# Optimization experiments

Hardware: AMD Instinct MI355X
Metric: run time of the kernel (lower is better)

Reference implementation:

```python
import jax, jax.numpy as jnp
import numpy as np


def _grid_sample_3d(vol, grid):
    """Trilinear 3D grid_sample, zero padding, align_corners=False (torch default).

    vol:  [B, C, D, H, W]
    grid: [B, P, 3] normalized coords in [-1, 1]; grid[...,0]->W axis,
          grid[...,1]->H axis, grid[...,2]->D axis (torch convention).
    returns [B, C, P]
    """
    B, C, D, H, W = vol.shape
    x = (grid[..., 0] + 1.0) * (W * 0.5) - 0.5
    y = (grid[..., 1] + 1.0) * (H * 0.5) - 0.5
    z = (grid[..., 2] + 1.0) * (D * 0.5) - 0.5
    x0, y0, z0 = jnp.floor(x), jnp.floor(y), jnp.floor(z)
    gather = jax.vmap(lambda v, zz, yy, xx: v[:, zz, yy, xx])  # per-batch gather -> [C, P]
    out = jnp.zeros((B, C, x.shape[1]), vol.dtype)
    for dz in (0.0, 1.0):
        for dy in (0.0, 1.0):
            for dx in (0.0, 1.0):
                xi, yi, zi = x0 + dx, y0 + dy, z0 + dz
                w = (1.0 - jnp.abs(x - xi)) * (1.0 - jnp.abs(y - yi)) * (1.0 - jnp.abs(z - zi))
                valid = (xi >= 0) & (xi < W) & (yi >= 0) & (yi < H) & (zi >= 0) & (zi < D)
                xc = jnp.clip(xi, 0, W - 1).astype(jnp.int32)
                yc = jnp.clip(yi, 0, H - 1).astype(jnp.int32)
                zc = jnp.clip(zi, 0, D - 1).astype(jnp.int32)
                vals = gather(vol, zc, yc, xc)  # [B, C, P]
                out = out + vals * jnp.where(valid, w, 0.0)[:, None, :]
    return out


def _offset_grid(xs, A, Wk):
    """xs: [N,3] sample points; A: [N,3,3]; Wk: [3,K] offset weights.
    Returns [N, K, 3] grid coords ordered (z_feat, y_feat, x_feat) as in the torch code."""
    off = jnp.einsum('nij,jk->nik', A, Wk)  # bmm with repeated weight -> [N,3,K]
    xf = xs[:, 2:3] + off[:, 0, :]
    yf = xs[:, 1:2] + off[:, 1, :]
    zf = xs[:, 0:1] + off[:, 2, :]
    return jnp.stack([zf, yf, xf], axis=-1)


def setup_inputs() -> dict:
    key = jax.random.key(0)
    k1, k2, k3, k4 = jax.random.split(key, 4)
    B, C, D, H, W = 2, 16, 96, 96, 96
    Feats, K = 512, 1024
    inp = jax.random.normal(k1, (B, C, D, H, W), jnp.float32)
    xyz_sample = jax.random.uniform(k2, (B, Feats, 3), jnp.float32, -1.0, 1.0)
    A = jax.random.normal(k3, (B * Feats, 3, 3), jnp.float32) * 0.1
    weight = jax.random.normal(k4, (6, K), jnp.float32) * 0.05  # xyz_off.weight
    return {"input": inp, "xyz_sample": xyz_sample, "A": A, "weight": weight}


def reference(input, xyz_sample, A, weight):
    B, Feats, _ = xyz_sample.shape
    C = input.shape[1]
    K = weight.shape[1]  # 1024
    xs = xyz_sample.reshape(B * Feats, 3)
    g1 = _offset_grid(xs, A, weight[:3]).reshape(B, Feats * K, 3)
    g2 = _offset_grid(xs, A, weight[3:]).reshape(B, Feats * K, 3)
    feats = _grid_sample_3d(input, g1) - _grid_sample_3d(input, g2)  # [B, C, Feats*K]
    return feats.reshape(B, C * Feats, K)
```

## Files before the change

kernel.cpp:

```cpp
#include <hip/hip_runtime.h>


#define NB 2
#define NC 16
#define NS 96
#define FEATS 512
#define NK 1024
#define KSPLIT 4
#define KSHIFT 2
#define KCHUNK (NK / KSPLIT)
#define PASSES (KCHUNK / 64)

#define TP 388

__device__ __forceinline__ unsigned int bfround(float f) {
  unsigned int u = __float_as_uint(f);
  return (u + 0x7fffu + ((u >> 16) & 1u)) >> 16;
}

__global__ __launch_bounds__(256) void transpose_bf16_kernel(
    const float* __restrict__ vol, unsigned short* __restrict__ volT) {
  int bid = blockIdx.x;
  int hq = bid % 24;
  int t = bid / 24;
  int d = t % NS;
  int b = t / NS;

  __shared__ float sm[NC * TP];
  int tid = threadIdx.x;

  const float4* v4 = (const float4*)vol;
#pragma unroll
  for (int j = 0; j < 6; j++) {
    int i = tid + 256 * j;
    int c = i / 96;
    int u = i - c * 96;
    size_t src = (size_t)((b * NC + c) * NS + d) * 2304 + hq * 96 + u;
    *(float4*)&sm[c * TP + u * 4] = v4[src];
  }
  __syncthreads();

  size_t dstb = ((size_t)(b * NS + d) * 9216 + (size_t)hq * 384) * NC;
#pragma unroll
  for (int j = 0; j < 3; j++) {
    int m = tid + 256 * j;
    int t16 = m >> 1;
    int ch = m & 1;
    unsigned int r[4];
#pragma unroll
    for (int q = 0; q < 4; q++) {
      float lo = sm[(ch * 8 + 2 * q) * TP + t16];
      float hi = sm[(ch * 8 + 2 * q + 1) * TP + t16];
      r[q] = bfround(lo) | (bfround(hi) << 16);
    }
    *(uint4*)(volT + dstb + (size_t)m * 8) = make_uint4(r[0], r[1], r[2], r[3]);
  }
}

__device__ __forceinline__ void tri_q_bf16(const unsigned short* __restrict__ vq,
                                           size_t bbase, float x, float y,
                                           float z, float sgn, float acc[4]) {
  float fx0 = floorf(x), fy0 = floorf(y), fz0 = floorf(z);
  int ix0 = (int)fx0, iy0 = (int)fy0, iz0 = (int)fz0;
  float tx = x - fx0, ty = y - fy0, tz = z - fz0;
  float wxa[2] = {1.0f - tx, tx};
  float wya[2] = {1.0f - ty, ty};
  float wza[2] = {1.0f - tz, tz};

#pragma unroll
  for (int dz = 0; dz < 2; dz++) {
    int zc = iz0 + dz;
    if ((unsigned)zc >= (unsigned)NS) continue;
#pragma unroll
    for (int dy = 0; dy < 2; dy++) {
      int yc = iy0 + dy;
      if ((unsigned)yc >= (unsigned)NS) continue;
      size_t rowb = bbase + ((size_t)zc * NS + yc) * (NS * NC);
      float wzy = sgn * wza[dz] * wya[dy];
#pragma unroll
      for (int dx = 0; dx < 2; dx++) {
        int xc = ix0 + dx;
        if ((unsigned)xc >= (unsigned)NS) continue;
        float w = wzy * wxa[dx];
        uint2 u = *(const uint2*)(vq + rowb + (size_t)xc * NC);
        acc[0] += w * __uint_as_float(u.x << 16);
        acc[1] += w * __uint_as_float(u.x & 0xffff0000u);
        acc[2] += w * __uint_as_float(u.y << 16);
        acc[3] += w * __uint_as_float(u.y & 0xffff0000u);
      }
    }
  }
}

__global__ __launch_bounds__(256) void sample_kernel_q(
    const unsigned short* __restrict__ volT,
    const float* __restrict__ xyz, const float* __restrict__ A,
    const float* __restrict__ weight, float* __restrict__ out) {
  __shared__ float wsm[6 * KCHUNK];

  int bid = blockIdx.x;
  int kseg = bid & (KSPLIT - 1);
  int n = bid >> KSHIFT;
  int b = n >> 9;
  int f = n & 511;
  int kbase = kseg * KCHUNK;

  for (int i = threadIdx.x; i < 6 * KCHUNK; i += 256)
    wsm[i] = weight[(i / KCHUNK) * NK + kbase + (i % KCHUNK)];

  const float* An = A + (size_t)n * 9;
  float a00 = An[0], a01 = An[1], a02 = An[2];
  float a10 = An[3], a11 = An[4], a12 = An[5];
  float a20 = An[6], a21 = An[7], a22 = An[8];
  const float* Xn = xyz + (size_t)n * 3;
  float bx = (Xn[0] + 1.0f) * 48.0f - 0.5f;
  float by = (Xn[1] + 1.0f) * 48.0f - 0.5f;
  float bz = (Xn[2] + 1.0f) * 48.0f - 0.5f;
  __syncthreads();

  int quad = threadIdx.x & 3;
  int ksub = threadIdx.x >> 2;
  const unsigned short* vq = volT + quad * 4;
  size_t bbase = (size_t)b * (NS * NS * NS * NC);
  size_t obase = (size_t)b * (NC * FEATS * NK) +
                 (size_t)(quad * 4) * (FEATS * NK) + (size_t)f * NK + kbase;

  for (int pass = 0; pass < PASSES; pass++) {
    int kl = pass * 64 + ksub;
    float w0 = wsm[kl];
    float w1 = wsm[KCHUNK + kl];
    float w2 = wsm[2 * KCHUNK + kl];
    float w3 = wsm[3 * KCHUNK + kl];
    float w4 = wsm[4 * KCHUNK + kl];
    float w5 = wsm[5 * KCHUNK + kl];

    float acc[4] = {0.0f, 0.0f, 0.0f, 0.0f};

    {
      float oz = a00 * w0 + a01 * w1 + a02 * w2;
      float oy = a10 * w0 + a11 * w1 + a12 * w2;
      float ox = a20 * w0 + a21 * w1 + a22 * w2;
      tri_q_bf16(vq, bbase, bx + ox * 48.0f, by + oy * 48.0f, bz + oz * 48.0f,
                 1.0f, acc);
    }
    {
      float oz = a00 * w3 + a01 * w4 + a02 * w5;
      float oy = a10 * w3 + a11 * w4 + a12 * w5;
      float ox = a20 * w3 + a21 * w4 + a22 * w5;
      tri_q_bf16(vq, bbase, bx + ox * 48.0f, by + oy * 48.0f, bz + oz * 48.0f,
                 -1.0f, acc);
    }

    size_t o = obase + kl;
    out[o] = acc[0];
    out[o + (size_t)(FEATS * NK)] = acc[1];
    out[o + 2 * (size_t)(FEATS * NK)] = acc[2];
    out[o + 3 * (size_t)(FEATS * NK)] = acc[3];
  }
}

__global__ __launch_bounds__(256) void sample_kernel_fallback(
    const float* __restrict__ vol, const float* __restrict__ xyz,
    const float* __restrict__ A, const float* __restrict__ weight,
    float* __restrict__ out) {
  int n = blockIdx.x;
  int b = n >> 9;
  int f = n & 511;
  const float* An = A + (size_t)n * 9;
  float a00 = An[0], a01 = An[1], a02 = An[2];
  float a10 = An[3], a11 = An[4], a12 = An[5];
  float a20 = An[6], a21 = An[7], a22 = An[8];
  const float* Xn = xyz + (size_t)n * 3;
  float bx = (Xn[0] + 1.0f) * 48.0f - 0.5f;
  float by = (Xn[1] + 1.0f) * 48.0f - 0.5f;
  float bz = (Xn[2] + 1.0f) * 48.0f - 0.5f;
  size_t obase = (size_t)b * (NC * FEATS * NK) + (size_t)f * NK;

  for (int k = threadIdx.x; k < NK; k += 256) {
    float w0 = weight[k], w1 = weight[NK + k], w2 = weight[2 * NK + k];
    float w3 = weight[3 * NK + k], w4 = weight[4 * NK + k],
          w5 = weight[5 * NK + k];
    float acc[NC];
#pragma unroll
    for (int c = 0; c < NC; c++) acc[c] = 0.0f;
    for (int g = 0; g < 2; g++) {
      float u0 = g ? w3 : w0, u1 = g ? w4 : w1, u2 = g ? w5 : w2;
      float sgn = g ? -1.0f : 1.0f;
      float oz = a00 * u0 + a01 * u1 + a02 * u2;
      float oy = a10 * u0 + a11 * u1 + a12 * u2;
      float ox = a20 * u0 + a21 * u1 + a22 * u2;
      float x = bx + ox * 48.0f, y = by + oy * 48.0f, z = bz + oz * 48.0f;
      float fx0 = floorf(x), fy0 = floorf(y), fz0 = floorf(z);
      int ix0 = (int)fx0, iy0 = (int)fy0, iz0 = (int)fz0;
      float tx = x - fx0, ty = y - fy0, tz = z - fz0;
      float wxa[2] = {1.0f - tx, tx}, wya[2] = {1.0f - ty, ty},
            wza[2] = {1.0f - tz, tz};
      for (int dz = 0; dz < 2; dz++) {
        int zc = iz0 + dz;
        if ((unsigned)zc >= (unsigned)NS) continue;
        for (int dy = 0; dy < 2; dy++) {
          int yc = iy0 + dy;
          if ((unsigned)yc >= (unsigned)NS) continue;
          for (int dx = 0; dx < 2; dx++) {
            int xc = ix0 + dx;
            if ((unsigned)xc >= (unsigned)NS) continue;
            float w = sgn * wza[dz] * wya[dy] * wxa[dx];
            size_t base = (size_t)b * NC * NS * NS * NS +
                          (size_t)zc * NS * NS + (size_t)yc * NS + xc;
#pragma unroll
            for (int c = 0; c < NC; c++)
              acc[c] += w * vol[base + (size_t)c * (NS * NS * NS)];
          }
        }
      }
    }
#pragma unroll
    for (int c = 0; c < NC; c++)
      out[obase + (size_t)c * (FEATS * NK) + k] = acc[c];
  }
}

extern "C" void kernel_launch(void* const* d_in, const int* in_sizes, int n_in,
                              void* d_out, int out_size, void* d_ws,
                              size_t ws_size, hipStream_t stream) {
  const float* vol    = (const float*)d_in[0];
  const float* xyz    = (const float*)d_in[1];
  const float* A      = (const float*)d_in[2];
  const float* weight = (const float*)d_in[3];
  float* out = (float*)d_out;

  const size_t volT_bytes =
      (size_t)NB * NC * NS * NS * NS * sizeof(unsigned short);

  if (ws_size >= volT_bytes) {
    unsigned short* volT = (unsigned short*)d_ws;
    transpose_bf16_kernel<<<NB * NS * 24, 256, 0, stream>>>(vol, volT);
    sample_kernel_q<<<NB * FEATS * KSPLIT, 256, 0, stream>>>(volT, xyz, A,
                                                             weight, out);
  } else {
    sample_kernel_fallback<<<NB * FEATS, 256, 0, stream>>>(vol, xyz, A, weight,
                                                           out);
  }
}
```

Before: 242.2 us.

## Stage local 8x8x8 voxel neighborhood in LDS and split channels across two threads

```diff
diff --git a/kernel.cpp b/kernel.cpp
--- a/kernel.cpp
+++ b/kernel.cpp
@@ -9,7 +9,10 @@
 #define KSPLIT 4
 #define KSHIFT 2
 #define KCHUNK (NK / KSPLIT)
-#define PASSES (KCHUNK / 64)
+#define DPASSES (KCHUNK / 128)
+
+#define RVOX 8
+#define VSTRIDE 48
 
 #define TP 388
 
@@ -57,9 +60,15 @@
   }
 }
 
-__device__ __forceinline__ void tri_q_bf16(const unsigned short* __restrict__ vq,
-                                           size_t bbase, float x, float y,
-                                           float z, float sgn, float acc[4]) {
+#define BLO(v) __uint_as_float((v) << 16)
+#define BHI(v) __uint_as_float((v) & 0xffff0000u)
+
+__device__ __forceinline__ void tri_duo(
+    const unsigned short* __restrict__ vg,
+    size_t bbase,
+    const unsigned char* __restrict__ sp,
+    int ox0, int oy0, int oz0,
+    float x, float y, float z, float sgn, float acc[8]) {
   float fx0 = floorf(x), fy0 = floorf(y), fz0 = floorf(z);
   int ix0 = (int)fx0, iy0 = (int)fy0, iz0 = (int)fz0;
   float tx = x - fx0, ty = y - fy0, tz = z - fz0;
@@ -67,26 +76,59 @@
   float wya[2] = {1.0f - ty, ty};
   float wza[2] = {1.0f - tz, tz};
 
-#pragma unroll
-  for (int dz = 0; dz < 2; dz++) {
-    int zc = iz0 + dz;
-    if ((unsigned)zc >= (unsigned)NS) continue;
-#pragma unroll
-    for (int dy = 0; dy < 2; dy++) {
-      int yc = iy0 + dy;
-      if ((unsigned)yc >= (unsigned)NS) continue;
-      size_t rowb = bbase + ((size_t)zc * NS + yc) * (NS * NC);
-      float wzy = sgn * wza[dz] * wya[dy];
-#pragma unroll
-      for (int dx = 0; dx < 2; dx++) {
-        int xc = ix0 + dx;
-        if ((unsigned)xc >= (unsigned)NS) continue;
-        float w = wzy * wxa[dx];
-        uint2 u = *(const uint2*)(vq + rowb + (size_t)xc * NC);
-        acc[0] += w * __uint_as_float(u.x << 16);
-        acc[1] += w * __uint_as_float(u.x & 0xffff0000u);
-        acc[2] += w * __uint_as_float(u.y << 16);
-        acc[3] += w * __uint_as_float(u.y & 0xffff0000u);
+  int lx0 = ix0 - ox0, ly0 = iy0 - oy0, lz0 = iz0 - oz0;
+  bool fast = ((unsigned)lx0 < 7u) & ((unsigned)ly0 < 7u) & ((unsigned)lz0 < 7u);
+
+  if (__builtin_expect(fast, 1)) {
+#pragma unroll
+    for (int dz = 0; dz < 2; dz++) {
+      float wz = sgn * wza[dz];
+#pragma unroll
+      for (int dy = 0; dy < 2; dy++) {
+        float wzy = wz * wya[dy];
+        const unsigned char* rp =
+            sp + (((lz0 + dz) * RVOX + (ly0 + dy)) * RVOX + lx0) * VSTRIDE;
+#pragma unroll
+        for (int dx = 0; dx < 2; dx++) {
+          float w = wzy * wxa[dx];
+          uint4 u = *(const uint4*)(rp + dx * VSTRIDE);
+          acc[0] += w * BLO(u.x);
+          acc[1] += w * BHI(u.x);
+          acc[2] += w * BLO(u.y);
+          acc[3] += w * BHI(u.y);
+          acc[4] += w * BLO(u.z);
+          acc[5] += w * BHI(u.z);
+          acc[6] += w * BLO(u.w);
+          acc[7] += w * BHI(u.w);
+        }
+      }
+    }
+  } else {
+#pragma unroll
+    for (int dz = 0; dz < 2; dz++) {
+      int zc = iz0 + dz;
+      if ((unsigned)zc >= (unsigned)NS) continue;
+#pragma unroll
+      for (int dy = 0; dy < 2; dy++) {
+        int yc = iy0 + dy;
+        if ((unsigned)yc >= (unsigned)NS) continue;
+        size_t rowb = bbase + ((size_t)zc * NS + yc) * (NS * NC);
+        float wzy = sgn * wza[dz] * wya[dy];
+#pragma unroll
+        for (int dx = 0; dx < 2; dx++) {
+          int xc = ix0 + dx;
+          if ((unsigned)xc >= (unsigned)NS) continue;
+          float w = wzy * wxa[dx];
+          uint4 u = *(const uint4*)(vg + rowb + (size_t)xc * NC);
+          acc[0] += w * BLO(u.x);
+          acc[1] += w * BHI(u.x);
+          acc[2] += w * BLO(u.y);
+          acc[3] += w * BHI(u.y);
+          acc[4] += w * BLO(u.z);
+          acc[5] += w * BHI(u.z);
+          acc[6] += w * BLO(u.w);
+          acc[7] += w * BHI(u.w);
+        }
       }
     }
   }
@@ -97,6 +139,7 @@
     const float* __restrict__ xyz, const float* __restrict__ A,
     const float* __restrict__ weight, float* __restrict__ out) {
   __shared__ float wsm[6 * KCHUNK];
+  __shared__ __align__(16) unsigned char stage[RVOX * RVOX * RVOX * VSTRIDE];
 
   int bid = blockIdx.x;
   int kseg = bid & (KSPLIT - 1);
@@ -116,17 +159,40 @@
   float bx = (Xn[0] + 1.0f) * 48.0f - 0.5f;
   float by = (Xn[1] + 1.0f) * 48.0f - 0.5f;
   float bz = (Xn[2] + 1.0f) * 48.0f - 0.5f;
+
+  int ox0 = (int)floorf(bx) - 3;
+  int oy0 = (int)floorf(by) - 3;
+  int oz0 = (int)floorf(bz) - 3;
+
+  size_t bbase = (size_t)b * (NS * NS * NS * NC);
+
+  for (int v = threadIdx.x; v < RVOX * RVOX * RVOX; v += 256) {
+    int dx = v & 7, dy = (v >> 3) & 7, dz = v >> 6;
+    int xc = ox0 + dx, yc = oy0 + dy, zc = oz0 + dz;
+    uint4 lo = make_uint4(0u, 0u, 0u, 0u);
+    uint4 hi = make_uint4(0u, 0u, 0u, 0u);
+    if (((unsigned)xc < (unsigned)NS) & ((unsigned)yc < (unsigned)NS) &
+        ((unsigned)zc < (unsigned)NS)) {
+      const uint4* g = (const uint4*)(volT + bbase +
+                                      (((size_t)zc * NS + yc) * NS + xc) * NC);
+      lo = g[0];
+      hi = g[1];
+    }
+    unsigned char* p = stage + (size_t)v * VSTRIDE;
+    *(uint4*)p = lo;
+    *(uint4*)(p + 16) = hi;
+  }
   __syncthreads();
 
-  int quad = threadIdx.x & 3;
-  int ksub = threadIdx.x >> 2;
-  const unsigned short* vq = volT + quad * 4;
-  size_t bbase = (size_t)b * (NS * NS * NS * NC);
+  int duo = threadIdx.x & 1;
+  int ksub = threadIdx.x >> 1;
+  const unsigned short* vg = volT + duo * 8;
+  const unsigned char* sp = stage + duo * 16;
   size_t obase = (size_t)b * (NC * FEATS * NK) +
-                 (size_t)(quad * 4) * (FEATS * NK) + (size_t)f * NK + kbase;
-
-  for (int pass = 0; pass < PASSES; pass++) {
-    int kl = pass * 64 + ksub;
+                 (size_t)(duo * 8) * (FEATS * NK) + (size_t)f * NK + kbase;
+
+  for (int pass = 0; pass < DPASSES; pass++) {
+    int kl = pass * 128 + ksub;
     float w0 = wsm[kl];
     float w1 = wsm[KCHUNK + kl];
     float w2 = wsm[2 * KCHUNK + kl];
@@ -134,28 +200,27 @@
     float w4 = wsm[4 * KCHUNK + kl];
     float w5 = wsm[5 * KCHUNK + kl];
 
-    float acc[4] = {0.0f, 0.0f, 0.0f, 0.0f};
+    float acc[8] = {0.0f, 0.0f, 0.0f, 0.0f, 0.0f, 0.0f, 0.0f, 0.0f};
 
     {
       float oz = a00 * w0 + a01 * w1 + a02 * w2;
       float oy = a10 * w0 + a11 * w1 + a12 * w2;
       float ox = a20 * w0 + a21 * w1 + a22 * w2;
-      tri_q_bf16(vq, bbase, bx + ox * 48.0f, by + oy * 48.0f, bz + oz * 48.0f,
-                 1.0f, acc);
+      tri_duo(vg, bbase, sp, ox0, oy0, oz0, bx + ox * 48.0f, by + oy * 48.0f,
+              bz + oz * 48.0f, 1.0f, acc);
     }
     {
       float oz = a00 * w3 + a01 * w4 + a02 * w5;
       float oy = a10 * w3 + a11 * w4 + a12 * w5;
       float ox = a20 * w3 + a21 * w4 + a22 * w5;
-      tri_q_bf16(vq, bbase, bx + ox * 48.0f, by + oy * 48.0f, bz + oz * 48.0f,
-                 -1.0f, acc);
+      tri_duo(vg, bbase, sp, ox0, oy0, oz0, bx + ox * 48.0f, by + oy * 48.0f,
+              bz + oz * 48.0f, -1.0f, acc);
     }
 
     size_t o = obase + kl;
-    out[o] = acc[0];
-    out[o + (size_t)(FEATS * NK)] = acc[1];
-    out[o + 2 * (size_t)(FEATS * NK)] = acc[2];
-    out[o + 3 * (size_t)(FEATS * NK)] = acc[3];
+#pragma unroll
+    for (int c = 0; c < 8; c++)
+      out[o + (size_t)c * (FEATS * NK)] = acc[c];
   }
 }
 
```

Measured after the change: 223.9 us. -7.6%, faster.
